# Optimization experiments

Measured on AMD Instinct MI355X. Metric: run time of the kernel, lower is better.

## Reference

```python
import jax, jax.numpy as jnp
import numpy as np

EPS = 1e-8        # LinearGELU eps
LN_EPS = 1e-5     # LayerNorm eps
NUM_HEADS = 16
DIM = 1024
HIDDEN = 4096
B, N = 4, 785


def _lin(x, xj, w, lw, b=None, lb=None):
    # LinearLinear: primal linear + JVP wrt input and tangent params (lw, lb)
    y = x @ w.T
    yj = xj @ w.T + x @ lw.T
    if b is not None:
        y = y + b
    if lb is not None:
        yj = yj + lb
    return y, yj


def _ln(x, xj, w, b, lw, lb):
    # LinearLayerNorm forward + manual JVP (matches torch source exactly)
    mean = x.mean(-1, keepdims=True)
    xc = x - mean
    var = (xc * xc).mean(-1, keepdims=True)
    std = jnp.sqrt(var + LN_EPS)
    xhat = xc / std
    out = xhat * w + b
    t1 = xhat * lw + lb                              # tangent wrt affine params
    mj = xj.mean(-1, keepdims=True)
    xjc = xj - mj
    a = xjc * std
    corr = 2.0 * (xc * xjc).mean(-1, keepdims=True)
    bterm = (0.5 / std) * corr * xc
    c = (1.0 / std) ** 2 * (a - bterm)
    return out, t1 + c * w


def _gelu(x, xj):
    # exact (erf) GELU; jvp uses gelu(x)/(x+EPS) + x*pdf(x) as in source
    out = 0.5 * x * (1.0 + jax.lax.erf(x * np.float32(1.0 / np.sqrt(2.0))))
    pdf = jnp.exp(-0.5 * x * x) * np.float32(1.0 / np.sqrt(2.0 * np.pi))
    return out, xj * (out / (x + EPS) + x * pdf)


def _attn(x, xj, qkv_w, qkv_lw, proj_w, proj_b, proj_lw, proj_lb):
    Bb, Nn, C = x.shape
    H = NUM_HEADS
    D = C // H
    scale = np.float32(D) ** -0.5
    qkv, qkv_j = _lin(x, xj, qkv_w, qkv_lw)  # [B,N,3C], qkv_bias=False
    def split(t):
        return t.reshape(Bb, Nn, 3, H, D).transpose(2, 0, 3, 1, 4)
    q, k, v = split(qkv)
    qj, kj, vj = split(qkv_j)
    q = q * scale
    qj = qj * scale
    attn = jax.nn.softmax(jnp.einsum('bhnd,bhmd->bhnm', q, k), axis=-1)
    out = jnp.einsum('bhnm,bhmd->bhnd', attn, v)
    # softmax JVP: dm = A_jvp + B_jvp; filter = dm*attn - rowsum(dm*attn)*attn
    dm = jnp.einsum('bhnd,bhmd->bhnm', qj, k) + jnp.einsum('bhnd,bhmd->bhnm', q, kj)
    f = dm * attn
    filt = f - f.sum(-1, keepdims=True) * attn  # == diag(dm @ attn^T) * attn correction
    out_j = jnp.einsum('bhnm,bhmd->bhnd', filt, v) + jnp.einsum('bhnm,bhmd->bhnd', attn, vj)
    out = out.transpose(0, 2, 1, 3).reshape(Bb, Nn, C)
    out_j = out_j.transpose(0, 2, 1, 3).reshape(Bb, Nn, C)
    return _lin(out, out_j, proj_w, proj_lw, proj_b, proj_lb)


def setup_inputs() -> dict:
    keys = jax.random.split(jax.random.key(0), 32)
    ki = iter(keys)
    def nrm(shape, s=0.02):
        return (jax.random.normal(next(ki), shape, jnp.float32) * s).astype(jnp.float32)
    d, h = DIM, HIDDEN
    inp = {
        'input': jax.random.normal(next(ki), (B, N, d), jnp.float32),
        'input_jvp': jax.random.normal(next(ki), (B, N, d), jnp.float32),
        'n1_w': 1.0 + nrm((d,), 0.1), 'n1_b': nrm((d,), 0.1),
        'n1_lw': nrm((d,), 0.1), 'n1_lb': nrm((d,), 0.1),
        'qkv_w': nrm((3 * d, d)), 'qkv_lw': nrm((3 * d, d)),
        'proj_w': nrm((d, d)), 'proj_b': nrm((d,), 0.1),
        'proj_lw': nrm((d, d)), 'proj_lb': nrm((d,), 0.1),
        'n2_w': 1.0 + nrm((d,), 0.1), 'n2_b': nrm((d,), 0.1),
        'n2_lw': nrm((d,), 0.1), 'n2_lb': nrm((d,), 0.1),
        'fc1_w': nrm((h, d)), 'fc1_b': nrm((h,), 0.1),
        'fc1_lw': nrm((h, d)), 'fc1_lb': nrm((h,), 0.1),
        'fc2_w': nrm((d, h)), 'fc2_b': nrm((d,), 0.1),
        'fc2_lw': nrm((d, h)), 'fc2_lb': nrm((d,), 0.1),
    }
    return inp


def reference(input, input_jvp, n1_w, n1_b, n1_lw, n1_lb, qkv_w, qkv_lw,
              proj_w, proj_b, proj_lw, proj_lb, n2_w, n2_b, n2_lw, n2_lb,
              fc1_w, fc1_b, fc1_lw, fc1_lb, fc2_w, fc2_b, fc2_lw, fc2_lb):
    x, xj = _ln(input, input_jvp, n1_w, n1_b, n1_lw, n1_lb)
    x, xj = _attn(x, xj, qkv_w, qkv_lw, proj_w, proj_b, proj_lw, proj_lb)
    x = x + input
    xj = xj + input_jvp
    i2, i2j = x, xj
    x, xj = _ln(x, xj, n2_w, n2_b, n2_lw, n2_lb)
    x, xj = _lin(x, xj, fc1_w, fc1_lw, fc1_b, fc1_lb)
    x, xj = _gelu(x, xj)
    x, xj = _lin(x, xj, fc2_w, fc2_lw, fc2_b, fc2_lb)
    return (x + i2, xj + i2j)
```

## Files before the change

### kernel.cpp

```cpp
#include <hip/hip_runtime.h>
#include <hip/hip_bf16.h>

typedef unsigned short u16;
typedef unsigned int   u32;

#define MP     3328
#define MREAL  3140
#define DIMC   1024
#define H3C    3072
#define HIDC   4096
#define NKV    785
#define SLEN   896

typedef __bf16 bf16x8 __attribute__((ext_vector_type(8)));
typedef float  f32x4  __attribute__((ext_vector_type(4)));

#define MFMA(d,a,b) (d) = __builtin_amdgcn_mfma_f32_16x16x32_bf16((a),(b),(d),0,0,0)

__device__ __forceinline__ u16 f2bf(float f){
  u32 u = __builtin_bit_cast(u32, f);
  return (u16)((u + 0x7fffu + ((u >> 16) & 1u)) >> 16);
}
__device__ __forceinline__ float bf2f(u16 h){
  return __builtin_bit_cast(float, (u32)h << 16);
}
__device__ __forceinline__ void gload16(const u16* g, u16* l){
  __builtin_amdgcn_global_load_lds(
      (const __attribute__((address_space(1))) void*)g,
      (__attribute__((address_space(3))) void*)l, 16, 0, 0);
}
__device__ __forceinline__ float wsum(float v){
  #pragma unroll
  for (int o = 32; o >= 1; o >>= 1) v += __shfl_xor(v, o);
  return v;
}

__global__ __launch_bounds__(256) void cvt2_k(
    const float* __restrict__ in0, u16* __restrict__ out0, int n0,
    const float* __restrict__ in1, u16* __restrict__ out1, int n1)
{
  int i = (blockIdx.x * 256 + threadIdx.x) * 4;
  const float* src; u16* dst;
  if (i < n0){ src = in0 + i; dst = out0 + i; }
  else { int j = i - n0; if (j >= n1) return; src = in1 + j; dst = out1 + j; }
  float4 v = *(const float4*)src;
  ushort4 o4;
  o4.x = f2bf(v.x); o4.y = f2bf(v.y); o4.z = f2bf(v.z); o4.w = f2bf(v.w);
  *(ushort4*)dst = o4;
}

__global__ __launch_bounds__(256) void ln_jvp_k(
    const float* __restrict__ x, const float* __restrict__ xj,
    const float* __restrict__ w, const float* __restrict__ b,
    const float* __restrict__ lw, const float* __restrict__ lb,
    u16* __restrict__ out, u16* __restrict__ outj)
{
  const int row = blockIdx.x, t = threadIdx.x;
  const size_t ro = (size_t)row * DIMC;
  if (row >= MREAL){
    for (int i = t; i < DIMC; i += 256){ out[ro+i] = 0; outj[ro+i] = 0; }
    return;
  }
  const float4 v  = ((const float4*)(x  + ro))[t];
  const float4 vj = ((const float4*)(xj + ro))[t];
  float sx  = v.x+v.y+v.z+v.w;
  float sxx = v.x*v.x+v.y*v.y+v.z*v.z+v.w*v.w;
  float sj  = vj.x+vj.y+vj.z+vj.w;
  float sxj = v.x*vj.x+v.y*vj.y+v.z*vj.z+v.w*vj.w;
  __shared__ __attribute__((aligned(64))) float red[4][4];
  sx = wsum(sx); sxx = wsum(sxx); sj = wsum(sj); sxj = wsum(sxj);
  const int wid = t>>6, lane = t&63;
  if (lane == 0){ red[wid][0]=sx; red[wid][1]=sxx; red[wid][2]=sj; red[wid][3]=sxj; }
  __syncthreads();
  sx  = red[0][0]+red[1][0]+red[2][0]+red[3][0];
  sxx = red[0][1]+red[1][1]+red[2][1]+red[3][1];
  sj  = red[0][2]+red[1][2]+red[2][2]+red[3][2];
  sxj = red[0][3]+red[1][3]+red[2][3]+red[3][3];
  const float inv  = 1.0f/1024.0f;
  const float mean = sx*inv, meanj = sj*inv;
  const float var  = sxx*inv - mean*mean;
  const float cov  = sxj*inv - mean*meanj;
  const float rstd = rsqrtf(var + 1e-5f);
  const float r3   = rstd*rstd*rstd;
  const float4 wv  = ((const float4*)w)[t];
  const float4 bv  = ((const float4*)b)[t];
  const float4 lwv = ((const float4*)lw)[t];
  const float4 lbv = ((const float4*)lb)[t];
  const float xs[4]  = {v.x,v.y,v.z,v.w},   xjs[4] = {vj.x,vj.y,vj.z,vj.w};
  const float wss[4] = {wv.x,wv.y,wv.z,wv.w}, bs[4] = {bv.x,bv.y,bv.z,bv.w};
  const float lws[4] = {lwv.x,lwv.y,lwv.z,lwv.w}, lbs[4] = {lbv.x,lbv.y,lbv.z,lbv.w};
  const int i0 = t*4;
  #pragma unroll
  for (int e = 0; e < 4; e++){
    const float xc = xs[e]-mean, xjc = xjs[e]-meanj;
    const float xhat = xc*rstd;
    const float cc = xjc*rstd - xc*cov*r3;
    out [ro+i0+e] = f2bf(xhat*wss[e] + bs[e]);
    outj[ro+i0+e] = f2bf(xhat*lws[e] + lbs[e] + cc*wss[e]);
  }
}

template<int EPI>
__global__ __launch_bounds__(512, 1) void gemm_jvp_wide_k(
    const u16* __restrict__ A, const u16* __restrict__ Aj, int lda,
    const u16* __restrict__ B, const u16* __restrict__ Bj, int K,
    const float* __restrict__ bias, const float* __restrict__ biasj,
    void* __restrict__ Yv, void* __restrict__ Yjv, int ldy)
{
  __shared__ __attribute__((aligned(128))) u16 lds[3][24576];
  const int tid = threadIdx.x, wid = tid>>6, lane = tid&63;
  const int l4 = lane>>4, l15 = lane&15;
  const int ord = blockIdx.y * gridDim.x + blockIdx.x;
  const int cpx = (gridDim.x * gridDim.y) >> 3;
  const int nbk = (ord & 7) * cpx + (ord >> 3);
  const int m0 = (nbk / gridDim.x) * 256;
  const int n0 = (nbk % gridDim.x) * 128;
  f32x4 accY[4][4], accJ[4][4];
  #pragma unroll
  for (int i = 0; i < 4; i++)
    #pragma unroll
    for (int j = 0; j < 4; j++){
      accY[i][j] = (f32x4){0.f,0.f,0.f,0.f};
      accJ[i][j] = (f32x4){0.f,0.f,0.f,0.f};
    }
  const int boA0 = tid*16,        boA1 = (512+tid)*16;
  const int sbA0 = boA0 ^ (((boA0>>7)&7)<<4);
  const int sbA1 = boA1 ^ (((boA1>>7)&7)<<4);
  const int rA0 = sbA0>>6, cA0 = (sbA0&63)>>1;
  const int rA1 = sbA1>>6, cA1 = (sbA1&63)>>1;
  const int boB = tid*16;
  const int sbB = boB ^ (((boB>>7)&7)<<4);
  const int rB = sbB>>6, cB = (sbB&63)>>1;
  const u16* srcA0  = A  + (size_t)(m0+rA0)*lda + cA0;
  const u16* srcA1  = A  + (size_t)(m0+rA1)*lda + cA1;
  const u16* srcAj0 = Aj + (size_t)(m0+rA0)*lda + cA0;
  const u16* srcAj1 = Aj + (size_t)(m0+rA1)*lda + cA1;
  const u16* srcB   = B  + (size_t)(n0+rB)*K + cB;
  const u16* srcBj  = Bj + (size_t)(n0+rB)*K + cB;
  const int dA0 = tid*8, dA1 = (512+tid)*8, dB = tid*8;
  const int wr = wid>>1, wc = wid&1;
  int aoff[4], boff[4];
  #pragma unroll
  for (int i = 0; i < 4; i++){
    int ab_ = (wr*64 + i*16 + l15)*64 + l4*16;
    aoff[i] = ab_ ^ (((ab_>>7)&7)<<4);
    int bb_ = (wc*64 + i*16 + l15)*64 + l4*16;
    boff[i] = bb_ ^ (((bb_>>7)&7)<<4);
  }
  auto STAGE = [&](int buf, int t){
    const int k0 = t<<5;
    u16* Lb = &lds[buf][0];
    gload16(srcA0 +k0, Lb + dA0);
    gload16(srcA1 +k0, Lb + dA1);
    gload16(srcAj0+k0, Lb + 8192 + dA0);
    gload16(srcAj1+k0, Lb + 8192 + dA1);
    gload16(srcB  +k0, Lb + 16384 + dB);
    gload16(srcBj +k0, Lb + 20480 + dB);
  };
  const int nt = K >> 5;
  STAGE(0, 0);
  STAGE(1, 1);
  for (int t = 0; t < nt; t++){
    if (t + 1 < nt) asm volatile("s_waitcnt vmcnt(6)" ::: "memory");
    else            asm volatile("s_waitcnt vmcnt(0)" ::: "memory");
    __builtin_amdgcn_s_barrier();
    if (t + 2 < nt) STAGE((t+2)%3, t+2);
    const char* Lb = (const char*)&lds[t%3][0];
    bf16x8 af[4], ajf[4], bbf[4], bjf[4];
    #pragma unroll
    for (int i = 0; i < 4; i++){
      af[i]  = *(const bf16x8*)(Lb + aoff[i]);
      ajf[i] = *(const bf16x8*)(Lb + 16384 + aoff[i]);
      bbf[i] = *(const bf16x8*)(Lb + 32768 + boff[i]);
      bjf[i] = *(const bf16x8*)(Lb + 40960 + boff[i]);
    }
    __builtin_amdgcn_s_setprio(1);
    #pragma unroll
    for (int i = 0; i < 4; i++)
      #pragma unroll
      for (int j = 0; j < 4; j++){
        MFMA(accY[i][j], af[i],  bbf[j]);
        MFMA(accJ[i][j], ajf[i], bbf[j]);
        MFMA(accJ[i][j], af[i],  bjf[j]);
      }
    __builtin_amdgcn_s_setprio(0);
  }
  const int mb = m0 + wr*64 + (l4<<2);
  const int nb = n0 + wc*64 + l15;
  #pragma unroll
  for (int i = 0; i < 4; i++)
    #pragma unroll
    for (int j = 0; j < 4; j++)
      #pragma unroll
      for (int r = 0; r < 4; r++){
        const int m = mb + i*16 + r, n = nb + j*16;
        float y = accY[i][j][r], yj = accJ[i][j][r];
        if (EPI == 0){
          ((u16*)Yv )[(size_t)m*ldy+n] = f2bf(y);
          ((u16*)Yjv)[(size_t)m*ldy+n] = f2bf(yj);
        } else {
          y  += bias[n];
          yj += biasj[n];
          const float ge  = 0.5f*y*(1.0f + erff(y*0.70710678118654752f));
          const float pdf = __expf(-0.5f*y*y)*0.3989422804014327f;
          const float gj  = yj*(ge/(y + 1e-8f) + y*pdf);
          ((u16*)Yv )[(size_t)m*ldy+n] = f2bf(ge);
          ((u16*)Yjv)[(size_t)m*ldy+n] = f2bf(gj);
        }
      }
}

template<int EPI>
__global__ __launch_bounds__(256) void gemm_jvp_k(
    const u16* __restrict__ A, const u16* __restrict__ Aj, int lda,
    const u16* __restrict__ B, const u16* __restrict__ Bj, int K,
    const float* __restrict__ bias, const float* __restrict__ biasj,
    const float* __restrict__ res, const float* __restrict__ resj,
    void* __restrict__ Yv, void* __restrict__ Yjv, int ldy, int mwrite)
{
  __shared__ __attribute__((aligned(128))) u16 lds[3][4][128*32];
  const int tid = threadIdx.x, wid = tid>>6, lane = tid&63;
  const int ord = blockIdx.y * gridDim.x + blockIdx.x;
  const int cpx = (gridDim.x * gridDim.y) >> 3;
  const int nbk = (ord & 7) * cpx + (ord >> 3);
  const int m0 = (nbk / gridDim.x) * 128;
  const int n0 = (nbk % gridDim.x) * 128;
  f32x4 accY[4][4], accJ[4][4];
  #pragma unroll
  for (int i = 0; i < 4; i++)
    #pragma unroll
    for (int j = 0; j < 4; j++){
      accY[i][j] = (f32x4){0.f,0.f,0.f,0.f};
      accJ[i][j] = (f32x4){0.f,0.f,0.f,0.f};
    }
  const int bo0 = wid*1024 + lane*16;
  const int bo1 = bo0 + 4096;
  const int sb0 = bo0 ^ (((bo0>>7)&7)<<4);
  const int sb1 = bo1 ^ (((bo1>>7)&7)<<4);
  const int r0 = sb0>>6, c0 = (sb0&63)>>1;
  const int r1 = sb1>>6, c1 = (sb1&63)>>1;
  const u16* A0  = A  + (size_t)(m0+r0)*lda + c0;
  const u16* A1  = A  + (size_t)(m0+r1)*lda + c1;
  const u16* Aj0 = Aj + (size_t)(m0+r0)*lda + c0;
  const u16* Aj1 = Aj + (size_t)(m0+r1)*lda + c1;
  const u16* B0  = B  + (size_t)(n0+r0)*K + c0;
  const u16* B1  = B  + (size_t)(n0+r1)*K + c1;
  const u16* Bj0 = Bj + (size_t)(n0+r0)*K + c0;
  const u16* Bj1 = Bj + (size_t)(n0+r1)*K + c1;
  const int kq = (lane>>4)<<3;
  const int ar = (wid>>1)*64 + (lane&15);
  const int bc = (wid&1)*64 + (lane&15);
  int aoff[4], boff[4];
  #pragma unroll
  for (int i = 0; i < 4; i++){
    int ab_ = (ar+i*16)*64 + (kq<<1);
    aoff[i] = ab_ ^ (((ab_>>7)&7)<<4);
    int bb_ = (bc+i*16)*64 + (kq<<1);
    boff[i] = bb_ ^ (((bb_>>7)&7)<<4);
  }
  auto STAGE = [&](int buf, int t){
    const int k0 = t<<5;
    u16* p0 = &lds[buf][0][0];
    gload16(A0 +k0, p0+(bo0>>1)); gload16(A1 +k0, p0+(bo1>>1));
    u16* p1 = &lds[buf][1][0];
    gload16(Aj0+k0, p1+(bo0>>1)); gload16(Aj1+k0, p1+(bo1>>1));
    u16* p2 = &lds[buf][2][0];
    gload16(B0 +k0, p2+(bo0>>1)); gload16(B1 +k0, p2+(bo1>>1));
    u16* p3 = &lds[buf][3][0];
    gload16(Bj0+k0, p3+(bo0>>1)); gload16(Bj1+k0, p3+(bo1>>1));
  };
  const int nt = K >> 5;
  STAGE(0, 0);
  STAGE(1, 1);
  for (int t = 0; t < nt; t++){
    if (t + 1 < nt) asm volatile("s_waitcnt vmcnt(8)" ::: "memory");
    else            asm volatile("s_waitcnt vmcnt(0)" ::: "memory");
    __builtin_amdgcn_s_barrier();
    if (t + 2 < nt) STAGE((t+2)%3, t+2);
    const char* lAb  = (const char*)&lds[t%3][0][0];
    const char* lAjb = (const char*)&lds[t%3][1][0];
    const char* lBb  = (const char*)&lds[t%3][2][0];
    const char* lBjb = (const char*)&lds[t%3][3][0];
    bf16x8 af[4], ajf[4], bbf[4], bjf[4];
    #pragma unroll
    for (int i = 0; i < 4; i++){
      af[i]  = *(const bf16x8*)(lAb  + aoff[i]);
      ajf[i] = *(const bf16x8*)(lAjb + aoff[i]);
      bbf[i] = *(const bf16x8*)(lBb  + boff[i]);
      bjf[i] = *(const bf16x8*)(lBjb + boff[i]);
    }
    __builtin_amdgcn_s_setprio(1);
    #pragma unroll
    for (int i = 0; i < 4; i++)
      #pragma unroll
      for (int j = 0; j < 4; j++){
        MFMA(accY[i][j], af[i],  bbf[j]);
        MFMA(accJ[i][j], ajf[i], bbf[j]);
        MFMA(accJ[i][j], af[i],  bjf[j]);
      }
    __builtin_amdgcn_s_setprio(0);
  }
  const int mb = m0 + (wid>>1)*64 + ((lane>>4)<<2);
  const int nb = n0 + (wid&1)*64 + (lane&15);
  #pragma unroll
  for (int i = 0; i < 4; i++)
    #pragma unroll
    for (int j = 0; j < 4; j++)
      #pragma unroll
      for (int r = 0; r < 4; r++){
        const int m = mb + i*16 + r, n = nb + j*16;
        float y = accY[i][j][r], yj = accJ[i][j][r];
        if (EPI == 0){
          ((u16*)Yv )[(size_t)m*ldy+n] = f2bf(y);
          ((u16*)Yjv)[(size_t)m*ldy+n] = f2bf(yj);
        } else if (EPI == 1){
          if (m < mwrite){
            y  += bias[n]  + res [(size_t)m*ldy+n];
            yj += biasj[n] + resj[(size_t)m*ldy+n];
            ((float*)Yv )[(size_t)m*ldy+n] = y;
            ((float*)Yjv)[(size_t)m*ldy+n] = yj;
          }
        } else {
          y  += bias[n];
          yj += biasj[n];
          const float ge  = 0.5f*y*(1.0f + erff(y*0.70710678118654752f));
          const float pdf = __expf(-0.5f*y*y)*0.3989422804014327f;
          const float gj  = yj*(ge/(y + 1e-8f) + y*pdf);
          ((u16*)Yv )[(size_t)m*ldy+n] = f2bf(ge);
          ((u16*)Yjv)[(size_t)m*ldy+n] = f2bf(gj);
        }
      }
}

__global__ __launch_bounds__(256) void transpose_v_k(
    const u16* __restrict__ qkvb, const u16* __restrict__ qkvjb,
    u16* __restrict__ vT, u16* __restrict__ vjT)
{
  __shared__ __attribute__((aligned(64))) u16 tl[64][80];
  __shared__ __attribute__((aligned(64))) u16 tlj[64][80];
  const int kt = blockIdx.x, bh = blockIdx.y;
  const int b = bh>>4, h = bh&15;
  const int t = threadIdx.x;
  const int kv = t>>2, dd = (t&3)*16;
  const int kvg = kt*64 + kv;
  if (kvg < NKV){
    const u16* s0 = qkvb  + (size_t)(b*NKV+kvg)*H3C + 2048 + h*64 + dd;
    const u16* s1 = qkvjb + (size_t)(b*NKV+kvg)*H3C + 2048 + h*64 + dd;
    *(uint4*)&tl [kv][dd]   = *(const uint4*)s0;
    *(uint4*)&tl [kv][dd+8] = *(const uint4*)(s0+8);
    *(uint4*)&tlj[kv][dd]   = *(const uint4*)s1;
    *(uint4*)&tlj[kv][dd+8] = *(const uint4*)(s1+8);
  } else {
    uint4 z = {0,0,0,0};
    *(uint4*)&tl [kv][dd] = z; *(uint4*)&tl [kv][dd+8] = z;
    *(uint4*)&tlj[kv][dd] = z; *(uint4*)&tlj[kv][dd+8] = z;
  }
  __syncthreads();
  const int d = t>>2, kc = (t&3)*16;
  u16* d0 = vT  + ((size_t)bh*64 + d)*SLEN + kt*64 + kc;
  u16* d1 = vjT + ((size_t)bh*64 + d)*SLEN + kt*64 + kc;
  #pragma unroll
  for (int e = 0; e < 16; e++){ d0[e] = tl[kc+e][d]; d1[e] = tlj[kc+e][d]; }
}

__global__ __launch_bounds__(256) void flash_attn_jvp_k(
    const u16* __restrict__ qkvb, const u16* __restrict__ qkvjb,
    const u16* __restrict__ vT, const u16* __restrict__ vjT,
    u16* __restrict__ o, u16* __restrict__ oj)
{
  __shared__ __attribute__((aligned(64))) u16 lK  [64*64];
  __shared__ __attribute__((aligned(64))) u16 lKj [64*64];
  __shared__ __attribute__((aligned(64))) u16 lvT [64*64];
  __shared__ __attribute__((aligned(64))) u16 lvjT[64*64];
  __shared__ __attribute__((aligned(64))) u16 pl  [128*64];
  __shared__ __attribute__((aligned(64))) u16 pdl [128*64];
  const int tid = threadIdx.x, wid = tid>>6, lane = tid&63;
  const int l4 = lane>>4, l15 = lane&15;
  const int qt = blockIdx.x, bh = blockIdx.y, b = bh>>4, h = bh&15;

  bf16x8 qf[2][2], qjf[2][2];
  {
    const size_t qrb = (size_t)b*NKV + qt*128 + wid*32;
    #pragma unroll
    for (int i = 0; i < 2; i++){
      const size_t ro = (qrb + i*16 + l15)*H3C + h*64;
      #pragma unroll
      for (int ks = 0; ks < 2; ks++){
        qf [i][ks] = *(const bf16x8*)(qkvb  + ro + ks*32 + l4*8);
        qjf[i][ks] = *(const bf16x8*)(qkvjb + ro + ks*32 + l4*8);
      }
    }
  }
  float m_st[2][4], l_st[2][4], g_st[2][4];
  f32x4 PO[2][4], PTJ[2][4];
  #pragma unroll
  for (int i = 0; i < 2; i++)
    #pragma unroll
    for (int r = 0; r < 4; r++){
      m_st[i][r] = -1e30f; l_st[i][r] = 0.f; g_st[i][r] = 0.f;
    }
  #pragma unroll
  for (int i = 0; i < 2; i++)
    #pragma unroll
    for (int j = 0; j < 4; j++){
      PO[i][j] = (f32x4){0.f,0.f,0.f,0.f};
      PTJ[i][j] = (f32x4){0.f,0.f,0.f,0.f};
    }
  const char* lKb   = (const char*)lK;
  const char* lKjb  = (const char*)lKj;
  const char* lvTb  = (const char*)lvT;
  const char* lvjTb = (const char*)lvjT;
  char* plb  = (char*)pl;
  char* pdlb = (char*)pdl;

  for (int t = 0; t < 13; t++){
    #pragma unroll
    for (int rnd = 0; rnd < 2; rnd++){
      const int gidx = rnd*256 + tid;
      const int row = gidx>>3, c = gidx&7;
      const int cs = c ^ (row&7);
      const size_t ksrc = (size_t)(b*NKV + t*64 + row)*H3C + 1024 + h*64 + cs*8;
      gload16(qkvb  + ksrc, lK  + gidx*8);
      gload16(qkvjb + ksrc, lKj + gidx*8);
      const size_t vsrc = ((size_t)bh*64 + row)*SLEN + t*64 + cs*8;
      gload16(vT  + vsrc, lvT  + gidx*8);
      gload16(vjT + vsrc, lvjT + gidx*8);
    }
    __syncthreads();

    #pragma unroll
    for (int i = 0; i < 2; i++){
      f32x4 s[4], dm[4];
      #pragma unroll
      for (int j = 0; j < 4; j++){
        s[j] = (f32x4){0.f,0.f,0.f,0.f};
        dm[j] = (f32x4){0.f,0.f,0.f,0.f};
      }
      #pragma unroll
      for (int ks = 0; ks < 2; ks++){
        #pragma unroll
        for (int j = 0; j < 4; j++){
          const int row = j*16 + l15;
          const int byt = (row*128 + ks*64 + l4*16) ^ ((row&7)<<4);
          const bf16x8 kf  = *(const bf16x8*)(lKb  + byt);
          const bf16x8 kjf = *(const bf16x8*)(lKjb + byt);
          MFMA(s[j],  qf[i][ks],  kf);
          MFMA(dm[j], qjf[i][ks], kf);
          MFMA(dm[j], qf[i][ks],  kjf);
        }
      }
      float tm[4] = {-1e30f,-1e30f,-1e30f,-1e30f};
      #pragma unroll
      for (int j = 0; j < 4; j++){
        const int colg = t*64 + j*16 + l15;
        #pragma unroll
        for (int r = 0; r < 4; r++){
          float sv = s[j][r]*0.125f;
          if (colg >= NKV) sv = -1e30f;
          s[j][r] = sv;
          dm[j][r] *= 0.125f;
          tm[r] = fmaxf(tm[r], sv);
        }
      }
      #pragma unroll
      for (int r = 0; r < 4; r++){
        float v = tm[r];
        v = fmaxf(v, __shfl_xor(v, 1));
        v = fmaxf(v, __shfl_xor(v, 2));
        v = fmaxf(v, __shfl_xor(v, 4));
        v = fmaxf(v, __shfl_xor(v, 8));
        const float mn = fmaxf(m_st[i][r], v);
        const float sc = __expf(m_st[i][r] - mn);
        m_st[i][r] = mn;
        l_st[i][r] *= sc;
        g_st[i][r] *= sc;
        #pragma unroll
        for (int j = 0; j < 4; j++){ PO[i][j][r] *= sc; PTJ[i][j][r] *= sc; }
      }
      float ps[4] = {0.f,0.f,0.f,0.f}, pds[4] = {0.f,0.f,0.f,0.f};
      #pragma unroll
      for (int j = 0; j < 4; j++){
        const int col = j*16 + l15;
        #pragma unroll
        for (int r = 0; r < 4; r++){
          const float p  = __expf(s[j][r] - m_st[i][r]);
          const float pd = p * dm[j][r];
          ps[r] += p; pds[r] += pd;
          const int row = wid*32 + i*16 + l4*4 + r;
          const int byt = (row*128 + col*2) ^ ((row&7)<<4);
          *(u16*)(plb  + byt) = f2bf(p);
          *(u16*)(pdlb + byt) = f2bf(pd);
        }
      }
      #pragma unroll
      for (int r = 0; r < 4; r++){
        float v = ps[r], w = pds[r];
        v += __shfl_xor(v, 1); w += __shfl_xor(w, 1);
        v += __shfl_xor(v, 2); w += __shfl_xor(w, 2);
        v += __shfl_xor(v, 4); w += __shfl_xor(w, 4);
        v += __shfl_xor(v, 8); w += __shfl_xor(w, 8);
        l_st[i][r] += v; g_st[i][r] += w;
      }
    }

    #pragma unroll
    for (int ks = 0; ks < 2; ks++){
      bf16x8 pa[2], pda[2];
      #pragma unroll
      for (int i = 0; i < 2; i++){
        const int row = wid*32 + i*16 + l15;
        const int byt = (row*128 + ks*64 + l4*16) ^ ((row&7)<<4);
        pa[i]  = *(const bf16x8*)(plb  + byt);
        pda[i] = *(const bf16x8*)(pdlb + byt);
      }
      #pragma unroll
      for (int j = 0; j < 4; j++){
        const int row = j*16 + l15;
        const int byt = (row*128 + ks*64 + l4*16) ^ ((row&7)<<4);
        const bf16x8 vb  = *(const bf16x8*)(lvTb  + byt);
        const bf16x8 vjb = *(const bf16x8*)(lvjTb + byt);
        #pragma unroll
        for (int i = 0; i < 2; i++){
          MFMA(PO[i][j],  pa[i],  vb);
          MFMA(PTJ[i][j], pda[i], vb);
          MFMA(PTJ[i][j], pa[i],  vjb);
        }
      }
    }
    __syncthreads();
  }

  #pragma unroll
  for (int i = 0; i < 2; i++)
    #pragma unroll
    for (int r = 0; r < 4; r++){
      const int ql = qt*128 + wid*32 + i*16 + l4*4 + r;
      if (ql < NKV){
        const float rl = 1.0f / l_st[i][r];
        const float gg = g_st[i][r] * rl;
        #pragma unroll
        for (int j = 0; j < 4; j++){
          const size_t oo = ((size_t)b*NKV + ql)*DIMC + h*64 + j*16 + l15;
          const float po = PO[i][j][r] * rl;
          o [oo] = f2bf(po);
          oj[oo] = f2bf(PTJ[i][j][r]*rl - gg*po);
        }
      }
    }
}

extern "C" void kernel_launch(void* const* d_in, const int* in_sizes, int n_in,
                              void* d_out, int out_size, void* d_ws, size_t ws_size,
                              hipStream_t stream)
{
  (void)in_sizes; (void)n_in; (void)out_size;
  const float* input   = (const float*)d_in[0];
  const float* inputj  = (const float*)d_in[1];
  const float* n1_w    = (const float*)d_in[2];
  const float* n1_b    = (const float*)d_in[3];
  const float* n1_lw   = (const float*)d_in[4];
  const float* n1_lb   = (const float*)d_in[5];
  const float* qkv_w   = (const float*)d_in[6];
  const float* qkv_lw  = (const float*)d_in[7];
  const float* proj_w  = (const float*)d_in[8];
  const float* proj_b  = (const float*)d_in[9];
  const float* proj_lw = (const float*)d_in[10];
  const float* proj_lb = (const float*)d_in[11];
  const float* n2_w    = (const float*)d_in[12];
  const float* n2_b    = (const float*)d_in[13];
  const float* n2_lw   = (const float*)d_in[14];
  const float* n2_lb   = (const float*)d_in[15];
  const float* fc1_w   = (const float*)d_in[16];
  const float* fc1_b   = (const float*)d_in[17];
  const float* fc1_lw  = (const float*)d_in[18];
  const float* fc1_lb  = (const float*)d_in[19];
  const float* fc2_w   = (const float*)d_in[20];
  const float* fc2_b   = (const float*)d_in[21];
  const float* fc2_lw  = (const float*)d_in[22];
  const float* fc2_lb  = (const float*)d_in[23];

  const size_t SZ_W      = 2u*4194304u*2u;
  const size_t SZ_ARENA1 = 2u*(size_t)MP*HIDC*2u;
  const size_t SZ_VT     = (size_t)64*64*SLEN*2u;
  const size_t SZ_ARENA2 = 2u*SZ_VT;
  const size_t SZ_ARENA3 = 2u*(size_t)MP*DIMC*2u;
  const size_t SZ_X2     = (size_t)MP*DIMC*4u;
  const size_t NEEDED = SZ_W + SZ_ARENA1 + SZ_ARENA2 + SZ_ARENA3 + 2u*SZ_X2 + 4096u;
  if (ws_size < NEEDED) return;

  char* base = (char*)d_ws;
  size_t off = 0;
  auto ab = [&](size_t bytes)->char*{
    char* p = base + off;
    off += bytes; off = (off + 255) & ~(size_t)255;
    return p;
  };
  char* Wslot  = ab(SZ_W);
  char* arena1 = ab(SZ_ARENA1);
  char* arena2 = ab(SZ_ARENA2);
  char* arena3 = ab(SZ_ARENA3);
  float* x2  = (float*)ab(SZ_X2);
  float* x2j = (float*)ab(SZ_X2);

  u16* wbuf  = (u16*)Wslot;
  u16* wjbuf = wbuf + 4194304;
  u16* qkvb  = (u16*)arena1;
  u16* qkvjb = qkvb + (size_t)MP*H3C;
  u16* hb    = (u16*)arena1;
  u16* hjb   = hb + (size_t)MP*HIDC;
  u16* vT    = (u16*)arena2;
  u16* vjT   = vT + (size_t)64*64*SLEN;
  u16* x3b   = (u16*)arena2;
  u16* x3jb  = x3b + (size_t)MP*DIMC;
  u16* x1b   = (u16*)arena3;
  u16* x1jb  = x1b + (size_t)MP*DIMC;
  u16* ob    = (u16*)arena3;
  u16* ojb   = ob + (size_t)MP*DIMC;

  auto cvt2 = [&](const float* s0, u16* d0, int n0,
                  const float* s1, u16* d1, int n1){
    cvt2_k<<<dim3((n0 + n1 + 1023)/1024), 256, 0, stream>>>(s0, d0, n0, s1, d1, n1);
  };

  ln_jvp_k<<<dim3(MP), 256, 0, stream>>>(input, inputj, n1_w, n1_b, n1_lw, n1_lb,
                                         x1b, x1jb);
  cvt2(qkv_w, wbuf, H3C*DIMC, qkv_lw, wjbuf, H3C*DIMC);
  gemm_jvp_wide_k<0><<<dim3(H3C/128, MP/256), 512, 0, stream>>>(
      x1b, x1jb, DIMC, wbuf, wjbuf, DIMC, nullptr, nullptr,
      qkvb, qkvjb, H3C);
  transpose_v_k<<<dim3(14, 64), 256, 0, stream>>>(qkvb, qkvjb, vT, vjT);
  flash_attn_jvp_k<<<dim3(7, 64), 256, 0, stream>>>(qkvb, qkvjb, vT, vjT, ob, ojb);
  cvt2(proj_w, wbuf, DIMC*DIMC, proj_lw, wjbuf, DIMC*DIMC);
  gemm_jvp_k<1><<<dim3(DIMC/128, MP/128), 256, 0, stream>>>(
      ob, ojb, DIMC, wbuf, wjbuf, DIMC, proj_b, proj_lb, input, inputj,
      x2, x2j, DIMC, MREAL);
  ln_jvp_k<<<dim3(MP), 256, 0, stream>>>(x2, x2j, n2_w, n2_b, n2_lw, n2_lb,
                                         x3b, x3jb);
  cvt2(fc1_w, wbuf, HIDC*DIMC, fc1_lw, wjbuf, HIDC*DIMC);
  gemm_jvp_wide_k<2><<<dim3(HIDC/128, MP/256), 512, 0, stream>>>(
      x3b, x3jb, DIMC, wbuf, wjbuf, DIMC, fc1_b, fc1_lb,
      hb, hjb, HIDC);
  cvt2(fc2_w, wbuf, DIMC*HIDC, fc2_lw, wjbuf, DIMC*HIDC);
  float* out0 = (float*)d_out;
  float* out1 = out0 + (size_t)MREAL*DIMC;
  gemm_jvp_k<1><<<dim3(DIMC/128, MP/128), 256, 0, stream>>>(
      hb, hjb, HIDC, wbuf, wjbuf, HIDC, fc2_b, fc2_lb, x2, x2j,
      out0, out1, DIMC, MREAL);
}
```

Measured before the change: 539.2 us.

## Double-buffer K tiles, lazy softmax rescale, defer row-sum reductions in flash attention JVP

Double-buffers the K/Kj shared tiles and issues the next tile's K loads and V loads asynchronously. Explicit vmcnt waits plus raw barriers let global loads overlap compute. The online-softmax rescale is skipped unless the running max grows by more than a threshold. Per-lane partial sums of p and p*dm are kept and reduced across lanes only once at the end, removing per-tile shuffles. This adds LDS usage and depends on hand-counted vmcnt values, and the lazy rescale lets exponentials grow to about e^4 before rescaling.

```diff
diff --git a/kernel.cpp b/kernel.cpp
--- a/kernel.cpp
+++ b/kernel.cpp
@@ -368,12 +368,12 @@
     const u16* __restrict__ vT, const u16* __restrict__ vjT,
     u16* __restrict__ o, u16* __restrict__ oj)
 {
-  __shared__ __attribute__((aligned(64))) u16 lK  [64*64];
-  __shared__ __attribute__((aligned(64))) u16 lKj [64*64];
-  __shared__ __attribute__((aligned(64))) u16 lvT [64*64];
-  __shared__ __attribute__((aligned(64))) u16 lvjT[64*64];
-  __shared__ __attribute__((aligned(64))) u16 pl  [128*64];
-  __shared__ __attribute__((aligned(64))) u16 pdl [128*64];
+  __shared__ __attribute__((aligned(128))) u16 lK  [2][64*64];
+  __shared__ __attribute__((aligned(128))) u16 lKj [2][64*64];
+  __shared__ __attribute__((aligned(128))) u16 lvT [64*64];
+  __shared__ __attribute__((aligned(128))) u16 lvjT[64*64];
+  __shared__ __attribute__((aligned(128))) u16 pl  [128*64];
+  __shared__ __attribute__((aligned(128))) u16 pdl [128*64];
   const int tid = threadIdx.x, wid = tid>>6, lane = tid&63;
   const int l4 = lane>>4, l15 = lane&15;
   const int qt = blockIdx.x, bh = blockIdx.y, b = bh>>4, h = bh&15;
@@ -391,13 +391,13 @@
       }
     }
   }
-  float m_st[2][4], l_st[2][4], g_st[2][4];
+  float m_st[2][4], l_pt[2][4], g_pt[2][4];
   f32x4 PO[2][4], PTJ[2][4];
   #pragma unroll
   for (int i = 0; i < 2; i++)
     #pragma unroll
     for (int r = 0; r < 4; r++){
-      m_st[i][r] = -1e30f; l_st[i][r] = 0.f; g_st[i][r] = 0.f;
+      m_st[i][r] = -1e30f; l_pt[i][r] = 0.f; g_pt[i][r] = 0.f;
     }
   #pragma unroll
   for (int i = 0; i < 2; i++)
@@ -406,27 +406,38 @@
       PO[i][j] = (f32x4){0.f,0.f,0.f,0.f};
       PTJ[i][j] = (f32x4){0.f,0.f,0.f,0.f};
     }
-  const char* lKb   = (const char*)lK;
-  const char* lKjb  = (const char*)lKj;
+  char* plb  = (char*)pl;
+  char* pdlb = (char*)pdl;
   const char* lvTb  = (const char*)lvT;
   const char* lvjTb = (const char*)lvjT;
-  char* plb  = (char*)pl;
-  char* pdlb = (char*)pdl;
-
+
+  const int g0 = tid, g1 = 256 + tid;
+  const int row0 = g0>>3, cs0 = (g0&7) ^ (row0&7);
+  const int row1 = g1>>3, cs1 = (g1&7) ^ (row1&7);
+  auto stageK = [&](int buf, int t){
+    const size_t k0 = (size_t)(b*NKV + t*64 + row0)*H3C + 1024 + h*64 + cs0*8;
+    const size_t k1 = (size_t)(b*NKV + t*64 + row1)*H3C + 1024 + h*64 + cs1*8;
+    gload16(qkvb  + k0, &lK [buf][0] + g0*8);
+    gload16(qkvjb + k0, &lKj[buf][0] + g0*8);
+    gload16(qkvb  + k1, &lK [buf][0] + g1*8);
+    gload16(qkvjb + k1, &lKj[buf][0] + g1*8);
+  };
+  auto stageV = [&](int t){
+    const size_t v0 = ((size_t)bh*64 + row0)*SLEN + t*64 + cs0*8;
+    const size_t v1 = ((size_t)bh*64 + row1)*SLEN + t*64 + cs1*8;
+    gload16(vT  + v0, lvT  + g0*8);
+    gload16(vjT + v0, lvjT + g0*8);
+    gload16(vT  + v1, lvT  + g1*8);
+    gload16(vjT + v1, lvjT + g1*8);
+  };
+
+  stageK(0, 0);
+  stageV(0);
   for (int t = 0; t < 13; t++){
-    #pragma unroll
-    for (int rnd = 0; rnd < 2; rnd++){
-      const int gidx = rnd*256 + tid;
-      const int row = gidx>>3, c = gidx&7;
-      const int cs = c ^ (row&7);
-      const size_t ksrc = (size_t)(b*NKV + t*64 + row)*H3C + 1024 + h*64 + cs*8;
-      gload16(qkvb  + ksrc, lK  + gidx*8);
-      gload16(qkvjb + ksrc, lKj + gidx*8);
-      const size_t vsrc = ((size_t)bh*64 + row)*SLEN + t*64 + cs*8;
-      gload16(vT  + vsrc, lvT  + gidx*8);
-      gload16(vjT + vsrc, lvjT + gidx*8);
-    }
-    __syncthreads();
+    asm volatile("s_waitcnt vmcnt(4)" ::: "memory");
+    __builtin_amdgcn_s_barrier();
+    const char* lKb  = (const char*)&lK [t&1][0];
+    const char* lKjb = (const char*)&lKj[t&1][0];
 
     #pragma unroll
     for (int i = 0; i < 2; i++){
@@ -462,6 +473,8 @@
           tm[r] = fmaxf(tm[r], sv);
         }
       }
+      float vmax[4];
+      bool need = false;
       #pragma unroll
       for (int r = 0; r < 4; r++){
         float v = tm[r];
@@ -469,15 +482,21 @@
         v = fmaxf(v, __shfl_xor(v, 2));
         v = fmaxf(v, __shfl_xor(v, 4));
         v = fmaxf(v, __shfl_xor(v, 8));
-        const float mn = fmaxf(m_st[i][r], v);
-        const float sc = __expf(m_st[i][r] - mn);
-        m_st[i][r] = mn;
-        l_st[i][r] *= sc;
-        g_st[i][r] *= sc;
+        vmax[r] = v;
+        need = need || (v > m_st[i][r] + 4.0f);
+      }
+      if (__any(need)){
         #pragma unroll
-        for (int j = 0; j < 4; j++){ PO[i][j][r] *= sc; PTJ[i][j][r] *= sc; }
-      }
-      float ps[4] = {0.f,0.f,0.f,0.f}, pds[4] = {0.f,0.f,0.f,0.f};
+        for (int r = 0; r < 4; r++){
+          const float nm = fmaxf(m_st[i][r], vmax[r]);
+          const float sc = __expf(m_st[i][r] - nm);
+          m_st[i][r] = nm;
+          l_pt[i][r] *= sc;
+          g_pt[i][r] *= sc;
+          #pragma unroll
+          for (int j = 0; j < 4; j++){ PO[i][j][r] *= sc; PTJ[i][j][r] *= sc; }
+        }
+      }
       #pragma unroll
       for (int j = 0; j < 4; j++){
         const int col = j*16 + l15;
@@ -485,23 +504,20 @@
         for (int r = 0; r < 4; r++){
           const float p  = __expf(s[j][r] - m_st[i][r]);
           const float pd = p * dm[j][r];
-          ps[r] += p; pds[r] += pd;
+          l_pt[i][r] += p;
+          g_pt[i][r] += pd;
           const int row = wid*32 + i*16 + l4*4 + r;
           const int byt = (row*128 + col*2) ^ ((row&7)<<4);
           *(u16*)(plb  + byt) = f2bf(p);
           *(u16*)(pdlb + byt) = f2bf(pd);
         }
       }
-      #pragma unroll
-      for (int r = 0; r < 4; r++){
-        float v = ps[r], w = pds[r];
-        v += __shfl_xor(v, 1); w += __shfl_xor(w, 1);
-        v += __shfl_xor(v, 2); w += __shfl_xor(w, 2);
-        v += __shfl_xor(v, 4); w += __shfl_xor(w, 4);
-        v += __shfl_xor(v, 8); w += __shfl_xor(w, 8);
-        l_st[i][r] += v; g_st[i][r] += w;
-      }
-    }
+    }
+
+    if (t + 1 < 13) stageK((t+1)&1, t+1);
+    if (t + 1 < 13) asm volatile("s_waitcnt vmcnt(4)" ::: "memory");
+    else            asm volatile("s_waitcnt vmcnt(0)" ::: "memory");
+    __builtin_amdgcn_s_barrier();
 
     #pragma unroll
     for (int ks = 0; ks < 2; ks++){
@@ -527,17 +543,23 @@
         }
       }
     }
-    __syncthreads();
+    __builtin_amdgcn_s_barrier();
+    if (t + 1 < 13) stageV(t+1);
   }
 
   #pragma unroll
   for (int i = 0; i < 2; i++)
     #pragma unroll
     for (int r = 0; r < 4; r++){
+      float lv = l_pt[i][r], gv = g_pt[i][r];
+      lv += __shfl_xor(lv, 1); gv += __shfl_xor(gv, 1);
+      lv += __shfl_xor(lv, 2); gv += __shfl_xor(gv, 2);
+      lv += __shfl_xor(lv, 4); gv += __shfl_xor(gv, 4);
+      lv += __shfl_xor(lv, 8); gv += __shfl_xor(gv, 8);
       const int ql = qt*128 + wid*32 + i*16 + l4*4 + r;
       if (ql < NKV){
-        const float rl = 1.0f / l_st[i][r];
-        const float gg = g_st[i][r] * rl;
+        const float rl = 1.0f / lv;
+        const float gg = gv * rl;
         #pragma unroll
         for (int j = 0; j < 4; j++){
           const size_t oo = ((size_t)b*NKV + ql)*DIMC + h*64 + j*16 + l15;
```

New measurement: 525.6 us. 2.5% less time.
